# Optimization experiments

Hardware: AMD Instinct MI355X
Metric: run time of the kernel (lower is better)

## Reference

```python
import jax, jax.numpy as jnp
import numpy as np

N = 50000      # nodes
E = 800000     # edges (before self loops)
IN = 128       # in_channels
H = 4          # heads
C = 32         # hidden_channels (per head)
D = H * C      # concat output dim = 128
NEG_SLOPE = 0.2
LN_EPS = 1e-5


def setup_inputs() -> dict:
    key = jax.random.key(0)
    ks = jax.random.split(key, 24)
    def p(k, shape, s=0.1):
        return jax.random.normal(k, shape, dtype=jnp.float32) * s
    inp = {
        "x": p(ks[0], (N, IN), 1.0),
        "edge_index": jax.random.randint(ks[1], (2, E), 0, N, dtype=jnp.int32),
    }
    i = 2
    for l, ind in [(0, IN), (1, D)]:
        inp[f"Wl{l}"] = p(ks[i], (ind, D)); i += 1
        inp[f"bl{l}"] = p(ks[i], (D,), 0.02); i += 1
        inp[f"Wr{l}"] = p(ks[i], (ind, D)); i += 1
        inp[f"br{l}"] = p(ks[i], (D,), 0.02); i += 1
        inp[f"att{l}"] = p(ks[i], (H, C)); i += 1
        inp[f"Wres{l}"] = p(ks[i], (ind, D)); i += 1
        inp[f"bias{l}"] = p(ks[i], (D,), 0.02); i += 1
        inp[f"g{l}"] = jnp.ones((D,), jnp.float32)
        inp[f"be{l}"] = jnp.zeros((D,), jnp.float32)
    return inp


def _gatv2_layer(x, src, dst, Wl, bl, Wr, br, att, Wres, bias):
    """GATv2Conv with concat heads, add_self_loops already applied, residual."""
    n = x.shape[0]
    xl = (x @ Wl + bl).reshape(n, H, C)   # source transform
    xr = (x @ Wr + br).reshape(n, H, C)   # target transform
    # edge-level attention logits: e = a . LeakyReLU(xl[j] + xr[i])  [E, H]
    eh = jax.nn.leaky_relu(xl[src] + xr[dst], negative_slope=NEG_SLOPE)  # [E,H,C]
    score = jnp.einsum('ehc,hc->eh', eh, att)                            # [E,H]
    # segment softmax over incoming edges of each destination node
    smax = jax.ops.segment_max(score, dst, num_segments=n)               # [N,H]
    ex = jnp.exp(score - smax[dst])
    ssum = jax.ops.segment_sum(ex, dst, num_segments=n)                  # [N,H]
    alpha = ex / ssum[dst]                                               # [E,H]
    msg = xl[src] * alpha[:, :, None]                                    # [E,H,C]
    out = jax.ops.segment_sum(msg, dst, num_segments=n).reshape(n, D)
    return out + x @ Wres + bias  # residual (bias=False linear) + final bias


def _layernorm_relu(x, g, b):
    mu = jnp.mean(x, axis=-1, keepdims=True)
    var = jnp.mean(jnp.square(x - mu), axis=-1, keepdims=True)
    return jax.nn.relu((x - mu) * jax.lax.rsqrt(var + LN_EPS) * g + b)


def reference(x, edge_index,
              Wl0, bl0, Wr0, br0, att0, Wres0, bias0, g0, be0,
              Wl1, bl1, Wr1, br1, att1, Wres1, bias1, g1, be1):
    n = x.shape[0]
    loops = jnp.arange(n, dtype=edge_index.dtype)
    src = jnp.concatenate([edge_index[0], loops])  # add_self_loops=True
    dst = jnp.concatenate([edge_index[1], loops])
    h = _gatv2_layer(x, src, dst, Wl0, bl0, Wr0, br0, att0, Wres0, bias0)
    h = _layernorm_relu(h, g0, be0)
    h = _gatv2_layer(h, src, dst, Wl1, bl1, Wr1, br1, att1, Wres1, bias1)
    h = _layernorm_relu(h, g1, be1)
    return h
```

## Files before the change

### kernel.cpp

```cpp
#include <hip/hip_runtime.h>
#include <math.h>

#define D 128
#define LRELU 0.2f
#define LN_EPS 1e-5f
#define INV_LN2 1.4426950408889634f

#define NBMAX 512
#define CAP 4096
#define P1CHUNK 8192

typedef __attribute__((ext_vector_type(8))) short short8;
typedef __attribute__((ext_vector_type(8))) unsigned short ushort8;
typedef __attribute__((ext_vector_type(4))) float f32x4;
typedef __attribute__((ext_vector_type(2))) float f32x2;
typedef __attribute__((ext_vector_type(2))) unsigned int u32x2;

static __device__ __forceinline__ unsigned short f2bf(float f) {
    union { float f; unsigned u; } a; a.f = f;
    unsigned r = a.u + 0x7FFFu + ((a.u >> 16) & 1u);
    return (unsigned short)(r >> 16);
}

static __device__ __forceinline__ f32x2 pk_add(f32x2 a, f32x2 b) {
    f32x2 d; asm("v_pk_add_f32 %0, %1, %2" : "=v"(d) : "v"(a), "v"(b)); return d;
}
static __device__ __forceinline__ f32x2 pk_mul(f32x2 a, f32x2 b) {
    f32x2 d; asm("v_pk_mul_f32 %0, %1, %2" : "=v"(d) : "v"(a), "v"(b)); return d;
}
static __device__ __forceinline__ f32x2 pk_fma(f32x2 a, f32x2 b, f32x2 c) {
    f32x2 d; asm("v_pk_fma_f32 %0, %1, %2, %3" : "=v"(d) : "v"(a), "v"(b), "v"(c)); return d;
}
static __device__ __forceinline__ f32x2 pk_abs(f32x2 a) {
    u32x2 u = __builtin_bit_cast(u32x2, a);
    u &= 0x7FFFFFFFu;
    return __builtin_bit_cast(f32x2, u);
}
static __device__ __forceinline__ f32x2 bf2x(unsigned u) {
    f32x2 r;
    r.x = __uint_as_float(u << 16);
    r.y = __uint_as_float(u & 0xFFFF0000u);
    return r;
}

static __device__ __forceinline__ float red4_dpp(float p) {
    int v = __builtin_amdgcn_update_dpp(0, __builtin_bit_cast(int, p), 0xB1, 0xf, 0xf, true);
    p += __builtin_bit_cast(float, v);
    v = __builtin_amdgcn_update_dpp(0, __builtin_bit_cast(int, p), 0x4E, 0xf, 0xf, true);
    p += __builtin_bit_cast(float, v);
    return p;
}

#define SCB 256


__global__ __launch_bounds__(256) void k_prep(
    const int* __restrict__ srcp, const int* __restrict__ dstp,
    int* __restrict__ bcur, unsigned* __restrict__ ebuf, int E, int N,
    const float* __restrict__ X, ushort* __restrict__ Xb, int Mp,
    const float* __restrict__ W0, const float* __restrict__ W1, const float* __restrict__ W2,
    const float* __restrict__ W3, const float* __restrict__ W4, const float* __restrict__ W5,
    ushort* __restrict__ Wp, int nP1, int nCV)
{
    const int bx = blockIdx.x;
    const int tid = threadIdx.x;
    if (bx < nP1) {
        __shared__ int h[NBMAX];
        const int E2 = E + N;
        const int e0 = bx * P1CHUNK;
        const int e1 = min(e0 + P1CHUNK, E2);
        for (int t = tid; t < NBMAX; t += 256) h[t] = 0;
        __syncthreads();
        for (int e = e0 + tid; e < e1; e += 256) {
            int d = (e < E) ? dstp[e] : e - E;
            atomicAdd(&h[d >> 7], 1);
        }
        __syncthreads();
        for (int b = tid; b < NBMAX; b += 256) {
            int c = h[b];
            h[b] = c ? atomicAdd(&bcur[b], c) : 0;
        }
        __syncthreads();
        for (int e = e0 + tid; e < e1; e += 256) {
            int d  = (e < E) ? dstp[e] : e - E;
            int sc = (e < E) ? srcp[e] : e - E;
            int b = d >> 7;
            int pos = atomicAdd(&h[b], 1) & (CAP - 1);
            ebuf[(size_t)b * CAP + pos] = ((unsigned)sc << 7) | (unsigned)(d & 127);
        }
    } else if (bx < nP1 + nCV) {
        int idx = (bx - nP1) * 256 + tid;
        if (idx >= Mp * (D / 4)) return;
        ushort4 o;
        if (idx < N * (D / 4)) {
            float4 v = ((const float4*)X)[idx];
            o.x = f2bf(v.x); o.y = f2bf(v.y); o.z = f2bf(v.z); o.w = f2bf(v.w);
        } else {
            o = make_ushort4(0, 0, 0, 0);
        }
        ((ushort4*)Xb)[idx] = o;
    } else {
        int bid = bx - nP1 - nCV;
        int m = bid >> 6;
        int o = ((bid & 63) << 8) + tid;
        const float* W;
        if (m == 0) W = W0; else if (m == 1) W = W1; else if (m == 2) W = W2;
        else if (m == 3) W = W3; else if (m == 4) W = W4; else W = W5;
        int j  = o & 7;
        int l  = (o >> 3) & 63;
        int ct = (o >> 9) & 7;
        int kc = o >> 12;
        int k   = kc * 32 + ((l >> 4) << 3) + j;
        int col = (ct << 4) + (l & 15);
        Wp[m * 16384 + o] = f2bf(W[k * D + col]);
    }
}


__global__ __launch_bounds__(256) void bhist_kernel(const unsigned* __restrict__ ebuf,
                                                    const int* __restrict__ bcur,
                                                    int* __restrict__ deg, int N) {
    const int b = blockIdx.x;
    const int base = b << 7;
    __shared__ int h[128];
    if (threadIdx.x < 128) h[threadIdx.x] = 0;
    __syncthreads();
    const int cnt = min(bcur[b], CAP);
    for (int k = threadIdx.x; k < cnt; k += 256) {
        unsigned v = ebuf[(size_t)b * CAP + k];
        atomicAdd(&h[v & 127], 1);
    }
    __syncthreads();
    if (threadIdx.x < 128 && base + threadIdx.x < N) deg[base + threadIdx.x] = h[threadIdx.x];
}


__global__ __launch_bounds__(SCB) void partial_kernel(const int* __restrict__ deg,
                                                      int* __restrict__ bsum, int n) {
    int i = blockIdx.x * SCB + threadIdx.x;
    int v = (i < n) ? deg[i] : 0;
    #pragma unroll
    for (int o = 32; o >= 1; o >>= 1) v += __shfl_xor(v, o);
    __shared__ int ws[4];
    if ((threadIdx.x & 63) == 0) ws[threadIdx.x >> 6] = v;
    __syncthreads();
    if (threadIdx.x == 0) bsum[blockIdx.x] = ws[0] + ws[1] + ws[2] + ws[3];
}

__global__ __launch_bounds__(SCB) void scan_bsum_kernel(int* __restrict__ bsum, int nb) {
    int t = threadIdx.x;
    int v = (t < nb) ? bsum[t] : 0;
    int incl = v;
    #pragma unroll
    for (int o = 1; o < 64; o <<= 1) {
        int u = __shfl_up(incl, o);
        if ((t & 63) >= o) incl += u;
    }
    __shared__ int wp[4];
    if ((t & 63) == 63) wp[t >> 6] = incl;
    __syncthreads();
    int add = 0;
    for (int k = 0; k < (t >> 6); ++k) add += wp[k];
    incl += add;
    if (t < nb) bsum[t] = incl - v;
}

__global__ __launch_bounds__(SCB) void write_off_kernel(const int* __restrict__ deg,
                                                        const int* __restrict__ boff,
                                                        int* __restrict__ off, int n) {
    int t = threadIdx.x;
    int i = blockIdx.x * SCB + t;
    int v = (i < n) ? deg[i] : 0;
    int incl = v;
    #pragma unroll
    for (int o = 1; o < 64; o <<= 1) {
        int u = __shfl_up(incl, o);
        if ((t & 63) >= o) incl += u;
    }
    __shared__ int wp[4];
    if ((t & 63) == 63) wp[t >> 6] = incl;
    __syncthreads();
    int add = boff[blockIdx.x];
    for (int k = 0; k < (t >> 6); ++k) add += wp[k];
    int excl = add + incl - v;
    if (i < n) off[i] = excl;
    if (i == n - 1) off[n] = excl + v;
}


static __device__ __forceinline__ void gemm_body(
    int bxg, int seg, int tid,
    const ushort* __restrict__ Xb, const ushort* __restrict__ Wp,
    const float* __restrict__ bl, const float* __restrict__ br,
    ushort* __restrict__ XLb, ushort* __restrict__ XRb, float* __restrict__ RES)
{
    const int l = tid & 63;
    const int wave = tid >> 6;
    const int wr = wave >> 1, wc = wave & 1;
    const int brow = bxg * 128 + wr * 64;
    const ushort* W = Wp + seg * 16384;

    f32x4 acc[4][4] = {};
    const int arow = brow + (l & 15);
    const int koff = (l >> 4) * 8;

    #pragma unroll
    for (int kc = 0; kc < 4; ++kc) {
        short8 A[4], B[4];
        #pragma unroll
        for (int at = 0; at < 4; ++at)
            A[at] = *(const short8*)&Xb[(size_t)(arow + at * 16) * D + kc * 32 + koff];
        #pragma unroll
        for (int ct = 0; ct < 4; ++ct) {
            int ctg = wc * 4 + ct;
            B[ct] = *(const short8*)&W[(((kc * 8 + ctg) * 64) + l) * 8];
        }
        #pragma unroll
        for (int at = 0; at < 4; ++at)
            #pragma unroll
            for (int ct = 0; ct < 4; ++ct)
                acc[at][ct] = __builtin_amdgcn_mfma_f32_16x16x32_bf16(A[at], B[ct], acc[at][ct], 0, 0, 0);
    }

    const int c = l & 15;
    const int r0 = (l >> 4) * 4;
    const float* bias = (seg == 0) ? bl : ((seg == 1) ? br : nullptr);
    #pragma unroll
    for (int ct = 0; ct < 4; ++ct) {
        int gcol = wc * 64 + ct * 16 + c;
        float bv = bias ? bias[gcol] : 0.f;
        #pragma unroll
        for (int at = 0; at < 4; ++at) {
            #pragma unroll
            for (int r = 0; r < 4; ++r) {
                int grow = brow + at * 16 + r0 + r;
                float v = acc[at][ct][r] + bv;
                size_t off = (size_t)grow * D + gcol;
                if (seg == 0)      XLb[off] = f2bf(v);
                else if (seg == 1) XRb[off] = f2bf(v);
                else               RES[off] = v;
            }
        }
    }
}


__global__ __launch_bounds__(256) void k_mid(
    const unsigned* __restrict__ ebuf, const int* __restrict__ bcur,
    const int* __restrict__ off, int* __restrict__ csrc, int N, int NB, int nblk,
    const ushort* __restrict__ Xb, const ushort* __restrict__ Wp,
    const float* __restrict__ bl, const float* __restrict__ br,
    ushort* __restrict__ XLb, ushort* __restrict__ XRb, float* __restrict__ RES)
{
    const int bx = blockIdx.x;
    if (bx < NB) {
        const int b = bx;
        const int base = b << 7;
        __shared__ int cur[128];
        if (threadIdx.x < 128)
            cur[threadIdx.x] = (base + threadIdx.x < N) ? off[base + threadIdx.x] : 0;
        __syncthreads();
        const int cnt = min(bcur[b], CAP);
        for (int k = threadIdx.x; k < cnt; k += 256) {
            unsigned v = ebuf[(size_t)b * CAP + k];
            int p = atomicAdd(&cur[v & 127], 1);
            csrc[p] = v >> 7;
        }
    } else {
        int bid = bx - NB;
        int seg = bid / nblk;
        int bxg = bid - seg * nblk;
        gemm_body(bxg, seg, threadIdx.x, Xb, Wp, bl, br, XLb, XRb, RES);
    }
}

__global__ __launch_bounds__(256) void gemm_mfma(
    const ushort* __restrict__ Xb, const ushort* __restrict__ Wp,
    const float* __restrict__ bl, const float* __restrict__ br,
    ushort* __restrict__ XLb, ushort* __restrict__ XRb, float* __restrict__ RES)
{
    gemm_body(blockIdx.x, blockIdx.y, threadIdx.x, Xb, Wp, bl, br, XLb, XRb, RES);
}


__global__ __launch_bounds__(256) void gat_node(
    const ushort* __restrict__ XLb, const ushort* __restrict__ XRb, const float* __restrict__ RES,
    const float* __restrict__ att, const float* __restrict__ bias,
    const float* __restrict__ g, const float* __restrict__ be,
    const int* __restrict__ off, const int* __restrict__ csrc,
    float* __restrict__ OUTf, ushort* __restrict__ OUTb)
{
    const int l = threadIdx.x & 63;
    const int i = blockIdx.x * 16 + (threadIdx.x >> 6) * 4 + (l >> 4);
    const int f = (l & 15) * 8;
    const unsigned ibase = ((unsigned)i << 7) + f;
    const int lb = l & 48;

    f32x2 at06[4], at04[4];
    #pragma unroll
    for (int k = 0; k < 4; ++k) {
        float2 a = *(const float2*)&att[f + k * 2];
        f32x2 av; av.x = a.x; av.y = a.y;
        at06[k] = av * (0.6f * INV_LN2);
        at04[k] = av * (0.4f * INV_LN2);
    }

    uint4 xru = *(const uint4*)&XRb[ibase];
    f32x2 xr2[4];
    xr2[0] = bf2x(xru.x); xr2[1] = bf2x(xru.y); xr2[2] = bf2x(xru.z); xr2[3] = bf2x(xru.w);

    const int e0 = off[i], e1 = off[i + 1];
    const int len = e1 - e0;
    int mx = max(len, __shfl_xor(len, 16));
    mx = max(mx, __shfl_xor(mx, 32));

    float m = -1e30f, s = 0.f;
    f32x2 a2[4] = {};

    for (int c0 = 0; c0 < mx; c0 += 16) {
        int myj = csrc[min(e0 + c0 + (l & 15), e1 - 1)];
        const int rem = mx - c0;
        const int kleft = len - c0;

        #pragma unroll
        for (int bb = 0; bb < 4; ++bb) {
            if (bb * 4 >= rem) break;
            int s0 = __shfl(myj, lb + bb * 4 + 0);
            int s1 = __shfl(myj, lb + bb * 4 + 1);
            int s2 = __shfl(myj, lb + bb * 4 + 2);
            int s3 = __shfl(myj, lb + bb * 4 + 3);
            uint4 u[4];
            u[0] = *(const uint4*)&XLb[((unsigned)s0 << 7) + f];
            u[1] = *(const uint4*)&XLb[((unsigned)s1 << 7) + f];
            u[2] = *(const uint4*)&XLb[((unsigned)s2 << 7) + f];
            u[3] = *(const uint4*)&XLb[((unsigned)s3 << 7) + f];

            const int kb = kleft - bb * 4;
            f32x2 xp[4][4];
            float p[4];
            #pragma unroll
            for (int j = 0; j < 4; ++j) {
                xp[j][0] = bf2x(u[j].x);
                xp[j][1] = bf2x(u[j].y);
                xp[j][2] = bf2x(u[j].z);
                xp[j][3] = bf2x(u[j].w);
                f32x2 v0 = pk_add(xp[j][0], xr2[0]);
                f32x2 pj2 = pk_mul(v0, at06[0]);
                pj2 = pk_fma(pk_abs(v0), at04[0], pj2);
                #pragma unroll
                for (int k = 1; k < 4; ++k) {
                    f32x2 v = pk_add(xp[j][k], xr2[k]);
                    pj2 = pk_fma(v, at06[k], pj2);
                    pj2 = pk_fma(pk_abs(v), at04[k], pj2);
                }
                float pj = pj2.x + pj2.y;
                pj = red4_dpp(pj);
                p[j] = (j < kb) ? pj : -1e30f;
            }
            float pmax = fmaxf(fmaxf(p[0], p[1]), fmaxf(p[2], p[3]));
            float nm = fmaxf(m, pmax);
            float so = exp2f(m - nm);
            float w0 = exp2f(p[0] - nm), w1 = exp2f(p[1] - nm);
            float w2 = exp2f(p[2] - nm), w3 = exp2f(p[3] - nm);
            s = s * so + ((w0 + w1) + (w2 + w3));
            f32x2 so2; so2.x = so; so2.y = so;
            f32x2 w02; w02.x = w0; w02.y = w0;
            f32x2 w12; w12.x = w1; w12.y = w1;
            f32x2 w22; w22.x = w2; w22.y = w2;
            f32x2 w32; w32.x = w3; w32.y = w3;
            #pragma unroll
            for (int k = 0; k < 4; ++k) {
                f32x2 t = pk_mul(xp[0][k], w02);
                t = pk_fma(xp[1][k], w12, t);
                t = pk_fma(xp[2][k], w22, t);
                t = pk_fma(xp[3][k], w32, t);
                a2[k] = pk_fma(a2[k], so2, t);
            }
            m = nm;
        }
    }

    const float4 rsA = *(const float4*)&RES[ibase];
    const float4 rsB = *(const float4*)&RES[ibase + 4];
    const float4 biA = *(const float4*)&bias[f];
    const float4 biB = *(const float4*)&bias[f + 4];
    float inv = 1.f / s;
    float r0 = a2[0].x * inv + rsA.x + biA.x;
    float r1 = a2[0].y * inv + rsA.y + biA.y;
    float r2 = a2[1].x * inv + rsA.z + biA.z;
    float r3 = a2[1].y * inv + rsA.w + biA.w;
    float r4 = a2[2].x * inv + rsB.x + biB.x;
    float r5 = a2[2].y * inv + rsB.y + biB.y;
    float r6 = a2[3].x * inv + rsB.z + biB.z;
    float r7 = a2[3].y * inv + rsB.w + biB.w;

    float sum = ((r0 + r1) + (r2 + r3)) + ((r4 + r5) + (r6 + r7));
    float sq  = ((r0 * r0 + r1 * r1) + (r2 * r2 + r3 * r3))
              + ((r4 * r4 + r5 * r5) + (r6 * r6 + r7 * r7));
    #pragma unroll
    for (int o = 8; o >= 1; o >>= 1) {
        sum += __shfl_xor(sum, o);
        sq  += __shfl_xor(sq, o);
    }
    float mu  = sum * (1.f / 128.f);
    float var = sq * (1.f / 128.f) - mu * mu;
    float isd = rsqrtf(var + LN_EPS);
    const float4 gvA = *(const float4*)&g[f];
    const float4 gvB = *(const float4*)&g[f + 4];
    const float4 bvA = *(const float4*)&be[f];
    const float4 bvB = *(const float4*)&be[f + 4];
    float o0 = fmaxf((r0 - mu) * isd * gvA.x + bvA.x, 0.f);
    float o1 = fmaxf((r1 - mu) * isd * gvA.y + bvA.y, 0.f);
    float o2 = fmaxf((r2 - mu) * isd * gvA.z + bvA.z, 0.f);
    float o3 = fmaxf((r3 - mu) * isd * gvA.w + bvA.w, 0.f);
    float o4 = fmaxf((r4 - mu) * isd * gvB.x + bvB.x, 0.f);
    float o5 = fmaxf((r5 - mu) * isd * gvB.y + bvB.y, 0.f);
    float o6 = fmaxf((r6 - mu) * isd * gvB.z + bvB.z, 0.f);
    float o7 = fmaxf((r7 - mu) * isd * gvB.w + bvB.w, 0.f);

    if (OUTb) {
        ushort8 ob;
        ob[0] = f2bf(o0); ob[1] = f2bf(o1); ob[2] = f2bf(o2); ob[3] = f2bf(o3);
        ob[4] = f2bf(o4); ob[5] = f2bf(o5); ob[6] = f2bf(o6); ob[7] = f2bf(o7);
        *(ushort8*)&OUTb[ibase] = ob;
    } else {
        *(float4*)&OUTf[ibase]     = make_float4(o0, o1, o2, o3);
        *(float4*)&OUTf[ibase + 4] = make_float4(o4, o5, o6, o7);
    }
}


extern "C" void kernel_launch(void* const* d_in, const int* in_sizes, int n_in,
                              void* d_out, int out_size, void* d_ws, size_t ws_size,
                              hipStream_t stream)
{
    const float* x    = (const float*)d_in[0];
    const int*   ei   = (const int*)d_in[1];
    const float* Wl0  = (const float*)d_in[2];
    const float* bl0  = (const float*)d_in[3];
    const float* Wr0  = (const float*)d_in[4];
    const float* br0  = (const float*)d_in[5];
    const float* att0 = (const float*)d_in[6];
    const float* Wres0= (const float*)d_in[7];
    const float* bias0= (const float*)d_in[8];
    const float* g0   = (const float*)d_in[9];
    const float* be0  = (const float*)d_in[10];
    const float* Wl1  = (const float*)d_in[11];
    const float* bl1  = (const float*)d_in[12];
    const float* Wr1  = (const float*)d_in[13];
    const float* br1  = (const float*)d_in[14];
    const float* att1 = (const float*)d_in[15];
    const float* Wres1= (const float*)d_in[16];
    const float* bias1= (const float*)d_in[17];
    const float* g1   = (const float*)d_in[18];
    const float* be1  = (const float*)d_in[19];

    const int N  = in_sizes[0] / D;
    const int E  = in_sizes[1] / 2;
    const int E2 = E + N;
    const int nblk = (N + 127) / 128;
    const int Mp = nblk * 128;
    const int nb = (N + SCB - 1) / SCB;
    const int NB = nblk;

    char* w = (char*)d_ws;
    ushort* Xb  = (ushort*)w; w += (size_t)Mp * D * 2;
    ushort* Hb  = (ushort*)w; w += (size_t)Mp * D * 2;
    ushort* XLb = (ushort*)w; w += (size_t)Mp * D * 2;
    ushort* XRb = (ushort*)w; w += (size_t)Mp * D * 2;
    float*  RES = (float*)w;  w += (size_t)Mp * D * 4;
    ushort* Wp  = (ushort*)w; w += (size_t)6 * 16384 * 2;
    int* deg     = (int*)w; w += (size_t)N * 4;
    int* off     = (int*)w; w += (size_t)(N + 1) * 4;
    int* bcur    = (int*)w; w += (size_t)NBMAX * 4;
    int* bsum    = (int*)w; w += (size_t)nb * 4;
    unsigned* ebuf = (unsigned*)w; w += (size_t)NB * CAP * 4;
    int* csrc    = (int*)w; w += (size_t)E2 * 4;

    const int* srcp = ei;
    const int* dstp = ei + E;

    const int nP1 = (E2 + P1CHUNK - 1) / P1CHUNK;
    const int nCV = (Mp * (D / 4) + 255) / 256;
    const int nPW = 6 * 64;
    const int nGM = nblk * 3;

    hipMemsetAsync(bcur, 0, (size_t)NBMAX * 4, stream);
    k_prep<<<nP1 + nCV + nPW, 256, 0, stream>>>(srcp, dstp, bcur, ebuf, E, N,
                                                x, Xb, Mp,
                                                Wl0, Wr0, Wres0, Wl1, Wr1, Wres1,
                                                Wp, nP1, nCV);
    bhist_kernel<<<NB, 256, 0, stream>>>(ebuf, bcur, deg, N);
    partial_kernel<<<nb, SCB, 0, stream>>>(deg, bsum, N);
    scan_bsum_kernel<<<1, SCB, 0, stream>>>(bsum, nb);
    write_off_kernel<<<nb, SCB, 0, stream>>>(deg, bsum, off, N);

    k_mid<<<NB + nGM, 256, 0, stream>>>(ebuf, bcur, off, csrc, N, NB, nblk,
                                        Xb, Wp, bl0, br0, XLb, XRb, RES);

    const int gatg = N / 16;
    dim3 ggrid(nblk, 3);

    gat_node<<<gatg, 256, 0, stream>>>(XLb, XRb, RES, att0, bias0, g0, be0, off, csrc, nullptr, Hb);
    gemm_mfma<<<ggrid, 256, 0, stream>>>(Hb, Wp + 3 * 16384, bl1, br1, XLb, XRb, RES);
    gat_node<<<gatg, 256, 0, stream>>>(XLb, XRb, RES, att1, bias1, g1, be1, off, csrc, (float*)d_out, nullptr);
}
```

Before: 191.1 us.

## Fuse degree scan into histogram and scatter kernels; prefetch neighbor rows in gather loop

The three-kernel prefix scan (partial sums, block scan, offset write) is removed. The histogram kernel now also writes a per-bucket total, and each scatter block in k_mid computes its own base offset by summing the preceding bucket totals, then scans its 128 local degrees. This cuts three kernel launches and their serialization. Separately, the GAT node aggregation loop now double-buffers neighbor feature loads, issuing the next group of four gathers before computing on the current one, to hide memory latency at the cost of extra registers.

```diff
diff --git a/kernel.cpp b/kernel.cpp
--- a/kernel.cpp
+++ b/kernel.cpp
@@ -50,8 +50,6 @@
     p += __builtin_bit_cast(float, v);
     return p;
 }
-
-#define SCB 256
 
 
 __global__ __launch_bounds__(256) void k_prep(
@@ -119,72 +117,29 @@
 
 __global__ __launch_bounds__(256) void bhist_kernel(const unsigned* __restrict__ ebuf,
                                                     const int* __restrict__ bcur,
-                                                    int* __restrict__ deg, int N) {
+                                                    int* __restrict__ deg,
+                                                    int* __restrict__ btot, int N) {
     const int b = blockIdx.x;
     const int base = b << 7;
+    const int tid = threadIdx.x;
     __shared__ int h[128];
-    if (threadIdx.x < 128) h[threadIdx.x] = 0;
+    __shared__ int t2[2];
+    if (tid < 128) h[tid] = 0;
     __syncthreads();
     const int cnt = min(bcur[b], CAP);
-    for (int k = threadIdx.x; k < cnt; k += 256) {
+    for (int k = tid; k < cnt; k += 256) {
         unsigned v = ebuf[(size_t)b * CAP + k];
         atomicAdd(&h[v & 127], 1);
     }
     __syncthreads();
-    if (threadIdx.x < 128 && base + threadIdx.x < N) deg[base + threadIdx.x] = h[threadIdx.x];
-}
-
-
-__global__ __launch_bounds__(SCB) void partial_kernel(const int* __restrict__ deg,
-                                                      int* __restrict__ bsum, int n) {
-    int i = blockIdx.x * SCB + threadIdx.x;
-    int v = (i < n) ? deg[i] : 0;
+    int v = (tid < 128) ? h[tid] : 0;
+    if (tid < 128 && base + tid < N) deg[base + tid] = v;
     #pragma unroll
     for (int o = 32; o >= 1; o >>= 1) v += __shfl_xor(v, o);
-    __shared__ int ws[4];
-    if ((threadIdx.x & 63) == 0) ws[threadIdx.x >> 6] = v;
+    if (tid == 0)  t2[0] = v;
+    if (tid == 64) t2[1] = v;
     __syncthreads();
-    if (threadIdx.x == 0) bsum[blockIdx.x] = ws[0] + ws[1] + ws[2] + ws[3];
-}
-
-__global__ __launch_bounds__(SCB) void scan_bsum_kernel(int* __restrict__ bsum, int nb) {
-    int t = threadIdx.x;
-    int v = (t < nb) ? bsum[t] : 0;
-    int incl = v;
-    #pragma unroll
-    for (int o = 1; o < 64; o <<= 1) {
-        int u = __shfl_up(incl, o);
-        if ((t & 63) >= o) incl += u;
-    }
-    __shared__ int wp[4];
-    if ((t & 63) == 63) wp[t >> 6] = incl;
-    __syncthreads();
-    int add = 0;
-    for (int k = 0; k < (t >> 6); ++k) add += wp[k];
-    incl += add;
-    if (t < nb) bsum[t] = incl - v;
-}
-
-__global__ __launch_bounds__(SCB) void write_off_kernel(const int* __restrict__ deg,
-                                                        const int* __restrict__ boff,
-                                                        int* __restrict__ off, int n) {
-    int t = threadIdx.x;
-    int i = blockIdx.x * SCB + t;
-    int v = (i < n) ? deg[i] : 0;
-    int incl = v;
-    #pragma unroll
-    for (int o = 1; o < 64; o <<= 1) {
-        int u = __shfl_up(incl, o);
-        if ((t & 63) >= o) incl += u;
-    }
-    __shared__ int wp[4];
-    if ((t & 63) == 63) wp[t >> 6] = incl;
-    __syncthreads();
-    int add = boff[blockIdx.x];
-    for (int k = 0; k < (t >> 6); ++k) add += wp[k];
-    int excl = add + incl - v;
-    if (i < n) off[i] = excl;
-    if (i == n - 1) off[n] = excl + v;
+    if (tid == 0) btot[b] = t2[0] + t2[1];
 }
 
 
@@ -247,7 +202,8 @@
 
 __global__ __launch_bounds__(256) void k_mid(
     const unsigned* __restrict__ ebuf, const int* __restrict__ bcur,
-    const int* __restrict__ off, int* __restrict__ csrc, int N, int NB, int nblk,
+    const int* __restrict__ deg, const int* __restrict__ btot,
+    int* __restrict__ off, int* __restrict__ csrc, int N, int NB, int nblk,
     const ushort* __restrict__ Xb, const ushort* __restrict__ Wp,
     const float* __restrict__ bl, const float* __restrict__ br,
     ushort* __restrict__ XLb, ushort* __restrict__ XRb, float* __restrict__ RES)
@@ -256,12 +212,43 @@
     if (bx < NB) {
         const int b = bx;
         const int base = b << 7;
+        const int tid = threadIdx.x;
         __shared__ int cur[128];
-        if (threadIdx.x < 128)
-            cur[threadIdx.x] = (base + threadIdx.x < N) ? off[base + threadIdx.x] : 0;
+        __shared__ int wsum[4];
+        __shared__ int wtot[2];
+
+        int acc = 0;
+        for (int t = tid; t < b; t += 256) acc += btot[t];
+        #pragma unroll
+        for (int o = 32; o >= 1; o >>= 1) acc += __shfl_xor(acc, o);
+        if ((tid & 63) == 0) wsum[tid >> 6] = acc;
         __syncthreads();
+        const int B = wsum[0] + wsum[1] + wsum[2] + wsum[3];
+
+        int dv = 0;
+        if (tid < 128 && base + tid < N) dv = deg[base + tid];
+        int incl = dv;
+        if (tid < 128) {
+            #pragma unroll
+            for (int o = 1; o < 64; o <<= 1) {
+                int u = __shfl_up(incl, o);
+                if ((tid & 63) >= o) incl += u;
+            }
+        }
+        if (tid == 63)  wtot[0] = incl;
+        if (tid == 127) wtot[1] = incl;
+        __syncthreads();
+        if (tid < 128) {
+            int add = (tid >= 64) ? wtot[0] : 0;
+            int excl = B + add + incl - dv;
+            cur[tid] = excl;
+            if (base + tid < N) off[base + tid] = excl;
+        }
+        if (b == NB - 1 && tid == 0) off[N] = B + wtot[0] + wtot[1];
+        __syncthreads();
+
         const int cnt = min(bcur[b], CAP);
-        for (int k = threadIdx.x; k < cnt; k += 256) {
+        for (int k = tid; k < cnt; k += 256) {
             unsigned v = ebuf[(size_t)b * CAP + k];
             int p = atomicAdd(&cur[v & 127], 1);
             csrc[p] = v >> 7;
@@ -320,30 +307,47 @@
     for (int c0 = 0; c0 < mx; c0 += 16) {
         int myj = csrc[min(e0 + c0 + (l & 15), e1 - 1)];
         const int rem = mx - c0;
+        const int nbb = min(4, (rem + 3) >> 2);
         const int kleft = len - c0;
+
+        uint4 u_[4];
+        {
+            int s0 = __shfl(myj, lb + 0);
+            int s1 = __shfl(myj, lb + 1);
+            int s2 = __shfl(myj, lb + 2);
+            int s3 = __shfl(myj, lb + 3);
+            u_[0] = *(const uint4*)&XLb[((unsigned)s0 << 7) + f];
+            u_[1] = *(const uint4*)&XLb[((unsigned)s1 << 7) + f];
+            u_[2] = *(const uint4*)&XLb[((unsigned)s2 << 7) + f];
+            u_[3] = *(const uint4*)&XLb[((unsigned)s3 << 7) + f];
+        }
 
         #pragma unroll
         for (int bb = 0; bb < 4; ++bb) {
-            if (bb * 4 >= rem) break;
-            int s0 = __shfl(myj, lb + bb * 4 + 0);
-            int s1 = __shfl(myj, lb + bb * 4 + 1);
-            int s2 = __shfl(myj, lb + bb * 4 + 2);
-            int s3 = __shfl(myj, lb + bb * 4 + 3);
-            uint4 u[4];
-            u[0] = *(const uint4*)&XLb[((unsigned)s0 << 7) + f];
-            u[1] = *(const uint4*)&XLb[((unsigned)s1 << 7) + f];
-            u[2] = *(const uint4*)&XLb[((unsigned)s2 << 7) + f];
-            u[3] = *(const uint4*)&XLb[((unsigned)s3 << 7) + f];
+            if (bb >= nbb) break;
+            uint4 uc[4];
+            #pragma unroll
+            for (int j = 0; j < 4; ++j) uc[j] = u_[j];
+            if (bb + 1 < nbb) {
+                int s0 = __shfl(myj, lb + (bb + 1) * 4 + 0);
+                int s1 = __shfl(myj, lb + (bb + 1) * 4 + 1);
+                int s2 = __shfl(myj, lb + (bb + 1) * 4 + 2);
+                int s3 = __shfl(myj, lb + (bb + 1) * 4 + 3);
+                u_[0] = *(const uint4*)&XLb[((unsigned)s0 << 7) + f];
+                u_[1] = *(const uint4*)&XLb[((unsigned)s1 << 7) + f];
+                u_[2] = *(const uint4*)&XLb[((unsigned)s2 << 7) + f];
+                u_[3] = *(const uint4*)&XLb[((unsigned)s3 << 7) + f];
+            }
 
             const int kb = kleft - bb * 4;
             f32x2 xp[4][4];
             float p[4];
             #pragma unroll
             for (int j = 0; j < 4; ++j) {
-                xp[j][0] = bf2x(u[j].x);
-                xp[j][1] = bf2x(u[j].y);
-                xp[j][2] = bf2x(u[j].z);
-                xp[j][3] = bf2x(u[j].w);
+                xp[j][0] = bf2x(uc[j].x);
+                xp[j][1] = bf2x(uc[j].y);
+                xp[j][2] = bf2x(uc[j].z);
+                xp[j][3] = bf2x(uc[j].w);
                 f32x2 v0 = pk_add(xp[j][0], xr2[0]);
                 f32x2 pj2 = pk_mul(v0, at06[0]);
                 pj2 = pk_fma(pk_abs(v0), at04[0], pj2);
@@ -460,7 +464,6 @@
     const int E2 = E + N;
     const int nblk = (N + 127) / 128;
     const int Mp = nblk * 128;
-    const int nb = (N + SCB - 1) / SCB;
     const int NB = nblk;
 
     char* w = (char*)d_ws;
@@ -473,7 +476,7 @@
     int* deg     = (int*)w; w += (size_t)N * 4;
     int* off     = (int*)w; w += (size_t)(N + 1) * 4;
     int* bcur    = (int*)w; w += (size_t)NBMAX * 4;
-    int* bsum    = (int*)w; w += (size_t)nb * 4;
+    int* btot    = (int*)w; w += (size_t)NBMAX * 4;
     unsigned* ebuf = (unsigned*)w; w += (size_t)NB * CAP * 4;
     int* csrc    = (int*)w; w += (size_t)E2 * 4;
 
@@ -490,12 +493,9 @@
                                                 x, Xb, Mp,
                                                 Wl0, Wr0, Wres0, Wl1, Wr1, Wres1,
                                                 Wp, nP1, nCV);
-    bhist_kernel<<<NB, 256, 0, stream>>>(ebuf, bcur, deg, N);
-    partial_kernel<<<nb, SCB, 0, stream>>>(deg, bsum, N);
-    scan_bsum_kernel<<<1, SCB, 0, stream>>>(bsum, nb);
-    write_off_kernel<<<nb, SCB, 0, stream>>>(deg, bsum, off, N);
-
-    k_mid<<<NB + nGM, 256, 0, stream>>>(ebuf, bcur, off, csrc, N, NB, nblk,
+    bhist_kernel<<<NB, 256, 0, stream>>>(ebuf, bcur, deg, btot, N);
+
+    k_mid<<<NB + nGM, 256, 0, stream>>>(ebuf, bcur, deg, btot, off, csrc, N, NB, nblk,
                                         Xb, Wp, bl0, br0, XLb, XRb, RES);
 
     const int gatg = N / 16;
```

Measured after the change: 183.1 us. 4.2% less time.
